# Optimization experiments

Hardware: AMD Instinct MI355X
Metric: run time of the kernel (lower is better)

Reference implementation:

```python
import jax, jax.numpy as jnp
import numpy as np

B, S, D, H, E, FF = 4, 1024, 1024, 16, 8, 2048
DH = D // H
EPS = 1e-5


def layer_norm(x, g, b):
    mu = jnp.mean(x, axis=-1, keepdims=True)
    var = jnp.mean(jnp.square(x - mu), axis=-1, keepdims=True)
    return (x - mu) * jax.lax.rsqrt(var + EPS) * g + b


def setup_inputs() -> dict:
    key = jax.random.key(0)
    ks = jax.random.split(key, 16)
    s = 1.0 / np.sqrt(D)
    sf = 1.0 / np.sqrt(FF)
    return {
        "src": jax.random.normal(ks[0], (B, S, D), jnp.float32),
        "src_key_padding_mask": jnp.zeros((B, S), jnp.bool_),
        "in_proj_w": jax.random.normal(ks[1], (3 * D, D), jnp.float32) * s,
        "in_proj_b": jnp.zeros((3 * D,), jnp.float32),
        "out_proj_w": jax.random.normal(ks[2], (D, D), jnp.float32) * s,
        "out_proj_b": jnp.zeros((D,), jnp.float32),
        "gate_w": jax.random.normal(ks[3], (E, D), jnp.float32) * s,
        "gate_b": jnp.zeros((E,), jnp.float32),
        "w1": jax.random.normal(ks[4], (E, D, FF), jnp.float32) * s,
        "b1": jnp.zeros((E, FF), jnp.float32),
        "w2": jax.random.normal(ks[5], (E, FF, D), jnp.float32) * sf,
        "b2": jnp.zeros((E, D), jnp.float32),
        "ln1_g": jnp.ones((D,), jnp.float32),
        "ln1_b": jnp.zeros((D,), jnp.float32),
        "ln2_g": jnp.ones((D,), jnp.float32),
        "ln2_b": jnp.zeros((D,), jnp.float32),
    }


def _encoder_layer(src, kpm, in_proj_w, in_proj_b, out_proj_w, out_proj_b,
                   gate_w, gate_b, w1, b1, w2, b2, ln1_g, ln1_b, ln2_g, ln2_b):
    # --- multi-head self-attention (batch_first, key_padding_mask) ---
    qkv = src @ in_proj_w.T + in_proj_b                       # [B,S,3D]
    q, k, v = jnp.split(qkv, 3, axis=-1)
    q = q.reshape(B, S, H, DH).transpose(0, 2, 1, 3)          # [B,H,S,DH]
    k = k.reshape(B, S, H, DH).transpose(0, 2, 1, 3)
    v = v.reshape(B, S, H, DH).transpose(0, 2, 1, 3)
    scores = jnp.einsum('bhqd,bhkd->bhqk', q, k) / np.sqrt(DH)
    scores = jnp.where(kpm[:, None, None, :], -jnp.inf, scores)
    attn = jax.nn.softmax(scores, axis=-1)
    ctx = jnp.einsum('bhqk,bhkd->bhqd', attn, v)              # [B,H,S,DH]
    ctx = ctx.transpose(0, 2, 1, 3).reshape(B, S, D)
    attn_out = ctx @ out_proj_w.T + out_proj_b

    x = layer_norm(src + attn_out, ln1_g, ln1_b)

    # --- MoE feedforward: softmax gate, dense weighted mixture of experts ---
    gates = jax.nn.softmax(x @ gate_w.T + gate_b, axis=-1)    # [B,S,E]
    h = jax.nn.relu(jnp.einsum('bsd,edf->bsef', x, w1) + b1)  # [B,S,E,FF]
    y = jnp.einsum('bsef,efd->bsed', h, w2) + b2              # [B,S,E,D]
    ff = jnp.einsum('bse,bsed->bsd', gates, y)

    return layer_norm(x + ff, ln2_g, ln2_b)


def reference(src, src_key_padding_mask, in_proj_w, in_proj_b, out_proj_w,
              out_proj_b, gate_w, gate_b, w1, b1, w2, b2,
              ln1_g, ln1_b, ln2_g, ln2_b):
    return _encoder_layer(src, src_key_padding_mask, in_proj_w, in_proj_b,
                          out_proj_w, out_proj_b, gate_w, gate_b,
                          w1, b1, w2, b2, ln1_g, ln1_b, ln2_g, ln2_b)
```

## Files before the change

kernel.cpp:

```cpp
#include <hip/hip_runtime.h>
#include <math.h>

#define B_   4
#define S_   1024
#define D_   1024
#define H_   16
#define DH_  64
#define E_   8
#define FF_  2048
#define M_   (B_ * S_)
#define EPS_ 1e-5f

typedef _Float16 f16;
typedef f16  f16x8 __attribute__((ext_vector_type(8)));
typedef f16  f16x4 __attribute__((ext_vector_type(4)));
typedef float f32x4 __attribute__((ext_vector_type(4)));

__device__ __forceinline__ void gl_lds16(const f16* g, f16* l) {
  __builtin_amdgcn_global_load_lds(
      (const __attribute__((address_space(1))) void*)g,
      (__attribute__((address_space(3))) void*)l, 16, 0, 0);
}

__global__ __launch_bounds__(256) void cvt_f16(
    const float* __restrict__ in, f16* __restrict__ out, int n8) {
  int i = blockIdx.x * 256 + threadIdx.x;
  if (i >= n8) return;
  float4 u = ((const float4*)in)[(size_t)i * 2];
  float4 v = ((const float4*)in)[(size_t)i * 2 + 1];
  f16x8 o;
  o[0] = (f16)u.x; o[1] = (f16)u.y; o[2] = (f16)u.z; o[3] = (f16)u.w;
  o[4] = (f16)v.x; o[5] = (f16)v.y; o[6] = (f16)v.z; o[7] = (f16)v.w;
  *(f16x8*)&out[(size_t)i * 8] = o;
}

__global__ __launch_bounds__(256) void transpose_cvt(
    const float* __restrict__ in, f16* __restrict__ out, int R, int C) {
  __shared__ float t[32][33];
  const size_t pl = (size_t)blockIdx.z * R * C;
  in += pl; out += pl;
  const int c0 = blockIdx.x * 32, r0 = blockIdx.y * 32;
  const int tx = threadIdx.x & 31, ty = threadIdx.x >> 5;
#pragma unroll
  for (int i = 0; i < 4; ++i)
    t[ty + 8 * i][tx] = in[(size_t)(r0 + ty + 8 * i) * C + c0 + tx];
  __syncthreads();
#pragma unroll
  for (int i = 0; i < 4; ++i)
    out[(size_t)(c0 + ty + 8 * i) * R + r0 + tx] = (f16)t[tx][ty + 8 * i];
}

#define MODE_F32  0
#define MODE_QKV  1
#define MODE_MOE1 2
#define MODE_MOE2 3

template<int MODE>
__global__ __launch_bounds__(256) void gemm16(
    const f16* __restrict__ A, const f16* __restrict__ B,
    const float* __restrict__ bias, const float* __restrict__ gates,
    float* __restrict__ Cf, f16* __restrict__ Ch,
    int N, int K, int e0, int ecnt, int accum) {
  __shared__ f16 Ah[128 * 64];
  __shared__ f16 Bh[128 * 64];
  const int tid = threadIdx.x;
  const int wid = tid >> 6, lane = tid & 63;
  const int wm = wid >> 1, wn = wid & 1;
  const int r16 = lane & 15, kg = lane >> 4;
  const int m0 = blockIdx.y * 128, n0 = blockIdx.x * 128;
  const int z = blockIdx.z;
  const int srow = lane >> 3;
  const int sslot = (lane & 7) ^ srow;

  const f16* Bb = B;
  f16* Chb = Ch;
  float* Cfb = Cf;
  if (MODE == MODE_MOE1) { Bb += (size_t)z * N * K; Chb += (size_t)z * M_ * N; }
  if (MODE == MODE_MOE2) { Cfb += (size_t)z * M_ * N; }

  char* AhB = (char*)Ah;
  char* BhB = (char*)Bh;
  const int rbA = (wm * 64 + r16) * 128;
  const int rbB = (wn * 64 + r16) * 128;
  const int sw0 = ((0 + kg) ^ (r16 & 7)) << 4;
  const int sw1 = ((4 + kg) ^ (r16 & 7)) << 4;

  f32x4 acc[4][4] = {};
  const int nloop = (MODE == MODE_MOE2) ? ecnt : 1;
  for (int ee = 0; ee < nloop; ++ee) {
    const f16* Ae = A;
    const f16* Be = Bb;
    if (MODE == MODE_MOE2) {
      Ae = A  + (size_t)(z * ecnt + ee) * M_ * K;
      Be = B  + (size_t)(z * ecnt + ee) * N * K;
    }
    const f16* ApL = Ae + (size_t)(m0 + wid * 32 + srow) * K + sslot * 8;
    const f16* BpL = Be + (size_t)(n0 + wid * 32 + srow) * K + sslot * 8;
    for (int k0 = 0; k0 < K; k0 += 64) {
      __syncthreads();
#pragma unroll
      for (int ia = 0; ia < 4; ++ia)
        gl_lds16(ApL + (size_t)ia * 8 * K + k0, (f16*)(AhB + (wid * 4 + ia) * 1024));
#pragma unroll
      for (int ib = 0; ib < 4; ++ib)
        gl_lds16(BpL + (size_t)ib * 8 * K + k0, (f16*)(BhB + (wid * 4 + ib) * 1024));
      __syncthreads();
#pragma unroll
      for (int ks = 0; ks < 2; ++ks) {
        const int sw = ks ? sw1 : sw0;
        f16x8 af[4], bf[4];
#pragma unroll
        for (int i = 0; i < 4; ++i)
          af[i] = *(const f16x8*)(AhB + rbA + i * 2048 + sw);
#pragma unroll
        for (int j = 0; j < 4; ++j)
          bf[j] = *(const f16x8*)(BhB + rbB + j * 2048 + sw);
#pragma unroll
        for (int i = 0; i < 4; ++i)
#pragma unroll
          for (int j = 0; j < 4; ++j)
            acc[i][j] = __builtin_amdgcn_mfma_f32_16x16x32_f16(
                af[i], bf[j], acc[i][j], 0, 0, 0);
      }
    }
  }
#pragma unroll
  for (int i = 0; i < 4; ++i) {
#pragma unroll
    for (int r = 0; r < 4; ++r) {
      const int row = m0 + wm * 64 + i * 16 + kg * 4 + r;
      float gsc = 0.f;
      if (MODE == MODE_MOE1) gsc = gates[(size_t)row * E_ + e0 + z];
#pragma unroll
      for (int j = 0; j < 4; ++j) {
        const int col = n0 + wn * 64 + j * 16 + r16;
        float v = acc[i][j][r];
        if (MODE == MODE_F32) {
          Cfb[(size_t)row * N + col] = v + bias[col];
        } else if (MODE == MODE_QKV) {
          Chb[(size_t)row * N + col] = (f16)(v + bias[col]);
        } else if (MODE == MODE_MOE1) {
          float t = fmaxf(v + bias[(size_t)(e0 + z) * N + col], 0.f) * gsc;
          Chb[(size_t)row * N + col] = (f16)t;
        } else {
          float o = v;
          if (accum) o += Cfb[(size_t)row * N + col];
          Cfb[(size_t)row * N + col] = o;
        }
      }
    }
  }
}

__global__ __launch_bounds__(256) void attn_kernel(
    const f16* __restrict__ qkv, const unsigned char* __restrict__ kpm,
    f16* __restrict__ ctxh) {
  __shared__ f16 Qs[64][72];
  __shared__ f16 Ks[64][72];
  __shared__ f16 VTs[64][72];
  __shared__ f16 Ps[4][16][72];
  const int tid = threadIdx.x;
  const int w = tid >> 6, lane = tid & 63;
  const int cx = lane & 15, qg = lane >> 4;
  const int qt = blockIdx.x, h = blockIdx.y, b = blockIdx.z;
  const size_t base = (size_t)b * S_ * (3 * D_);
  const f16* Qg = qkv + base + h * 64;
  const f16* Kg = qkv + base + D_ + h * 64;
  const f16* Vg = qkv + base + 2 * D_ + h * 64;
  const int lr = tid >> 2, lc = (tid & 3) * 16;

  {
    const f16* sp = &Qg[(size_t)(qt * 64 + lr) * (3 * D_) + lc];
    *(f16x8*)&Qs[lr][lc]     = *(const f16x8*)&sp[0];
    *(f16x8*)&Qs[lr][lc + 8] = *(const f16x8*)&sp[8];
  }
  __syncthreads();
  f16x8 aq0 = *(const f16x8*)&Qs[w * 16 + cx][qg * 8];
  f16x8 aq1 = *(const f16x8*)&Qs[w * 16 + cx][32 + qg * 8];

  f32x4 accO[4] = {};
  float mrun[4], lrun[4];
#pragma unroll
  for (int r = 0; r < 4; ++r) { mrun[r] = -__builtin_inff(); lrun[r] = 0.f; }

  for (int kt = 0; kt < 16; ++kt) {
    __syncthreads();
    {
      const f16* ksp = &Kg[(size_t)(kt * 64 + lr) * (3 * D_) + lc];
      const f16* vsp = &Vg[(size_t)(kt * 64 + lr) * (3 * D_) + lc];
      *(f16x8*)&Ks[lr][lc]     = *(const f16x8*)&ksp[0];
      *(f16x8*)&Ks[lr][lc + 8] = *(const f16x8*)&ksp[8];
      f16x8 v0 = *(const f16x8*)&vsp[0];
      f16x8 v1 = *(const f16x8*)&vsp[8];
#pragma unroll
      for (int j = 0; j < 8; ++j) {
        VTs[lc + j][lr]     = v0[j];
        VTs[lc + 8 + j][lr] = v1[j];
      }
    }
    __syncthreads();
    f32x4 s[4];
#pragma unroll
    for (int t = 0; t < 4; ++t) {
      f16x8 bk0 = *(const f16x8*)&Ks[t * 16 + cx][qg * 8];
      f16x8 bk1 = *(const f16x8*)&Ks[t * 16 + cx][32 + qg * 8];
      f32x4 zz = {};
      zz = __builtin_amdgcn_mfma_f32_16x16x32_f16(aq0, bk0, zz, 0, 0, 0);
      zz = __builtin_amdgcn_mfma_f32_16x16x32_f16(aq1, bk1, zz, 0, 0, 0);
      s[t] = zz;
    }
    const unsigned char* mp = &kpm[(size_t)b * S_ + kt * 64];
    bool mk[4];
#pragma unroll
    for (int t = 0; t < 4; ++t) mk[t] = mp[t * 16 + cx] != 0;
#pragma unroll
    for (int r = 0; r < 4; ++r) {
      float sv[4];
#pragma unroll
      for (int t = 0; t < 4; ++t)
        sv[t] = mk[t] ? -__builtin_inff() : s[t][r] * 0.125f;
      float mx = fmaxf(fmaxf(sv[0], sv[1]), fmaxf(sv[2], sv[3]));
#pragma unroll
      for (int mm = 1; mm < 16; mm <<= 1) mx = fmaxf(mx, __shfl_xor(mx, mm, 64));
      float mnew = fmaxf(mrun[r], mx);
      float al = (mrun[r] == -__builtin_inff()) ? 0.f : __expf(mrun[r] - mnew);
      float ps = 0.f;
#pragma unroll
      for (int t = 0; t < 4; ++t) {
        float p = __expf(sv[t] - mnew);
        Ps[w][qg * 4 + r][t * 16 + cx] = (f16)p;
        ps += p;
      }
#pragma unroll
      for (int mm = 1; mm < 16; mm <<= 1) ps += __shfl_xor(ps, mm, 64);
      lrun[r] = lrun[r] * al + ps;
      mrun[r] = mnew;
#pragma unroll
      for (int t = 0; t < 4; ++t) accO[t][r] *= al;
    }
    f16x8 ap0 = *(const f16x8*)&Ps[w][cx][qg * 8];
    f16x8 ap1 = *(const f16x8*)&Ps[w][cx][32 + qg * 8];
#pragma unroll
    for (int td = 0; td < 4; ++td) {
      f16x8 bv0 = *(const f16x8*)&VTs[td * 16 + cx][qg * 8];
      f16x8 bv1 = *(const f16x8*)&VTs[td * 16 + cx][32 + qg * 8];
      accO[td] = __builtin_amdgcn_mfma_f32_16x16x32_f16(ap0, bv0, accO[td], 0, 0, 0);
      accO[td] = __builtin_amdgcn_mfma_f32_16x16x32_f16(ap1, bv1, accO[td], 0, 0, 0);
    }
  }
  f16* outp = ctxh + (size_t)b * S_ * D_ + h * 64;
#pragma unroll
  for (int r = 0; r < 4; ++r) {
    float inv = 1.f / lrun[r];
    const size_t rofs = (size_t)(qt * 64 + w * 16 + qg * 4 + r) * D_;
#pragma unroll
    for (int td = 0; td < 4; ++td)
      outp[rofs + td * 16 + cx] = (f16)(accO[td][r] * inv);
  }
}

__global__ __launch_bounds__(256) void add_ln(
    const float* __restrict__ x1, const float* __restrict__ parts, int nparts,
    const float* __restrict__ gates, const float* __restrict__ b2,
    const float* __restrict__ g, const float* __restrict__ bta,
    float* __restrict__ out, f16* __restrict__ outh) {
  __shared__ float red[4];
  const int row = blockIdx.x, tid = threadIdx.x;
  const size_t off = (size_t)row * D_ + tid * 4;
  float4 a = *(const float4*)&x1[off];
  float v[4] = {a.x, a.y, a.z, a.w};
  for (int p = 0; p < nparts; ++p) {
    float4 c = *(const float4*)&parts[(size_t)p * M_ * D_ + off];
    v[0] += c.x; v[1] += c.y; v[2] += c.z; v[3] += c.w;
  }
  if (gates) {
#pragma unroll
    for (int e = 0; e < E_; ++e) {
      float ge = gates[(size_t)row * E_ + e];
      float4 bb = *(const float4*)&b2[(size_t)e * D_ + tid * 4];
      v[0] += ge * bb.x; v[1] += ge * bb.y; v[2] += ge * bb.z; v[3] += ge * bb.w;
    }
  }
  float p = v[0] + v[1] + v[2] + v[3];
#pragma unroll
  for (int mm = 32; mm >= 1; mm >>= 1) p += __shfl_xor(p, mm, 64);
  if ((tid & 63) == 0) red[tid >> 6] = p;
  __syncthreads();
  float mu = (red[0] + red[1] + red[2] + red[3]) * (1.f / D_);
  __syncthreads();
  float d0 = v[0] - mu, d1 = v[1] - mu, d2 = v[2] - mu, d3 = v[3] - mu;
  float p2 = d0 * d0 + d1 * d1 + d2 * d2 + d3 * d3;
#pragma unroll
  for (int mm = 32; mm >= 1; mm >>= 1) p2 += __shfl_xor(p2, mm, 64);
  if ((tid & 63) == 0) red[tid >> 6] = p2;
  __syncthreads();
  float var = (red[0] + red[1] + red[2] + red[3]) * (1.f / D_);
  float sc = rsqrtf(var + EPS_);
  float4 gg = *(const float4*)&g[tid * 4];
  float4 bb = *(const float4*)&bta[tid * 4];
  float o0 = d0 * sc * gg.x + bb.x;
  float o1 = d1 * sc * gg.y + bb.y;
  float o2 = d2 * sc * gg.z + bb.z;
  float o3 = d3 * sc * gg.w + bb.w;
  float4 o = {o0, o1, o2, o3};
  *(float4*)&out[off] = o;
  if (outh) {
    f16x4 oh; oh[0] = (f16)o0; oh[1] = (f16)o1; oh[2] = (f16)o2; oh[3] = (f16)o3;
    *(f16x4*)&outh[off] = oh;
  }
}

__global__ __launch_bounds__(256) void gate_kernel(
    const float* __restrict__ x, const float* __restrict__ gw,
    const float* __restrict__ gb, float* __restrict__ gates) {
  const int lane = threadIdx.x & 63;
  const int row = blockIdx.x * 4 + (threadIdx.x >> 6);
  const float* xr = x + (size_t)row * D_;
  float a[E_] = {};
#pragma unroll
  for (int c = 0; c < 4; ++c) {
    float4 xv = *(const float4*)&xr[lane * 16 + c * 4];
#pragma unroll
    for (int e = 0; e < E_; ++e) {
      float4 wv = *(const float4*)&gw[(size_t)e * D_ + lane * 16 + c * 4];
      a[e] += xv.x * wv.x + xv.y * wv.y + xv.z * wv.z + xv.w * wv.w;
    }
  }
#pragma unroll
  for (int e = 0; e < E_; ++e) {
#pragma unroll
    for (int mm = 1; mm < 64; mm <<= 1) a[e] += __shfl_xor(a[e], mm, 64);
    a[e] += gb[e];
  }
  if (lane == 0) {
    float mx = a[0];
#pragma unroll
    for (int e = 1; e < E_; ++e) mx = fmaxf(mx, a[e]);
    float pr[E_], sum = 0.f;
#pragma unroll
    for (int e = 0; e < E_; ++e) { pr[e] = __expf(a[e] - mx); sum += pr[e]; }
    float inv = 1.f / sum;
#pragma unroll
    for (int e = 0; e < E_; ++e) gates[(size_t)row * E_ + e] = pr[e] * inv;
  }
}

extern "C" void kernel_launch(void* const* d_in, const int* in_sizes, int n_in,
                              void* d_out, int out_size, void* d_ws, size_t ws_size,
                              hipStream_t stream) {
  (void)in_sizes; (void)n_in; (void)out_size;
  const float* src         = (const float*)d_in[0];
  const unsigned char* kpm = (const unsigned char*)d_in[1];
  const float* in_proj_w   = (const float*)d_in[2];
  const float* in_proj_b   = (const float*)d_in[3];
  const float* out_proj_w  = (const float*)d_in[4];
  const float* out_proj_b  = (const float*)d_in[5];
  const float* gate_w      = (const float*)d_in[6];
  const float* gate_b      = (const float*)d_in[7];
  const float* w1          = (const float*)d_in[8];
  const float* b1          = (const float*)d_in[9];
  const float* w2          = (const float*)d_in[10];
  const float* b2          = (const float*)d_in[11];
  const float* ln1_g       = (const float*)d_in[12];
  const float* ln1_b       = (const float*)d_in[13];
  const float* ln2_g       = (const float*)d_in[14];
  const float* ln2_b       = (const float*)d_in[15];
  float* out = (float*)d_out;

  const size_t MD4 = (size_t)M_ * D_ * 4;
  const size_t MD2 = (size_t)M_ * D_ * 2;
  const size_t persist = MD4 + MD2 + (size_t)M_ * E_ * 4;
  const size_t wfull   = (size_t)E_ * D_ * FF_ * 2;
  const size_t phaseA  = MD2 + (size_t)3 * D_ * D_ * 2 + (size_t)D_ * D_ * 2
                       + (size_t)M_ * 3 * D_ * 2 + MD2 + MD4;
  const size_t phaseBb = (size_t)E_ * M_ * FF_ * 2 + 4 * MD4;
  const size_t bigBytes = persist + 2 * wfull + (phaseBb > phaseA ? phaseBb : phaseA);

  char* p = (char*)d_ws;
  float* x_  = (float*)p;  p += MD4;
  f16*   x_h = (f16*)p;    p += MD2;
  float* gts = (float*)p;  p += (size_t)M_ * E_ * 4;
  const bool big = ws_size >= bigBytes;
  f16 *w1t = nullptr, *w2t = nullptr;
  if (big) { w1t = (f16*)p; p += wfull; w2t = (f16*)p; p += wfull; }
  char* region = p;
  f16*   src_h = (f16*)region;
  f16*   ipw   = (f16*)(region + MD2);
  f16*   opw   = (f16*)(region + MD2 + 6291456);
  f16*   qkvh  = (f16*)(region + MD2 + 6291456 + 2097152);
  f16*   ctxh  = (f16*)(region + MD2 + 6291456 + 2097152 + 25165824);
  float* aout  = (float*)(region + MD2 + 6291456 + 2097152 + 25165824 + MD2);

  dim3 blk(256);
  cvt_f16<<<2048, blk, 0, stream>>>(src, src_h, M_ * D_ / 8);
  cvt_f16<<<1536, blk, 0, stream>>>(in_proj_w, ipw, 3 * D_ * D_ / 8);
  cvt_f16<<<512,  blk, 0, stream>>>(out_proj_w, opw, D_ * D_ / 8);
  if (big) {
    transpose_cvt<<<dim3(FF_ / 32, D_ / 32, E_), blk, 0, stream>>>(w1, w1t, D_, FF_);
    transpose_cvt<<<dim3(D_ / 32, FF_ / 32, E_), blk, 0, stream>>>(w2, w2t, FF_, D_);
  }
  gemm16<MODE_QKV><<<dim3(24, 32), blk, 0, stream>>>(
      src_h, ipw, in_proj_b, nullptr, nullptr, qkvh, 3 * D_, D_, 0, 0, 0);
  attn_kernel<<<dim3(S_ / 64, H_, B_), blk, 0, stream>>>(qkvh, kpm, ctxh);
  gemm16<MODE_F32><<<dim3(8, 32), blk, 0, stream>>>(
      ctxh, opw, out_proj_b, nullptr, aout, nullptr, D_, D_, 0, 0, 0);
  add_ln<<<M_, blk, 0, stream>>>(src, aout, 1, nullptr, nullptr, ln1_g, ln1_b, x_, x_h);
  gate_kernel<<<M_ / 4, blk, 0, stream>>>(x_, gate_w, gate_b, gts);
  if (big) {
    f16*   h_h = (f16*)region;
    float* ff  = (float*)(region + (size_t)E_ * M_ * FF_ * 2);
    gemm16<MODE_MOE1><<<dim3(16, 32, 8), blk, 0, stream>>>(
        x_h, w1t, b1, gts, nullptr, h_h, FF_, D_, 0, 0, 0);
    gemm16<MODE_MOE2><<<dim3(8, 32, 4), blk, 0, stream>>>(
        h_h, w2t, nullptr, nullptr, ff, nullptr, D_, FF_, 0, 2, 0);
    add_ln<<<M_, blk, 0, stream>>>(x_, ff, 4, gts, b2, ln2_g, ln2_b, out, nullptr);
  } else {
    f16*   w1tp = (f16*)region;
    f16*   w2tp = (f16*)(region + 8388608);
    f16*   h_p  = (f16*)(region + 16777216);
    float* ffp  = (float*)(region + 16777216 + 33554432);
    for (int pp = 0; pp < 4; ++pp) {
      transpose_cvt<<<dim3(FF_ / 32, D_ / 32, 2), blk, 0, stream>>>(
          w1 + (size_t)pp * 2 * D_ * FF_, w1tp, D_, FF_);
      transpose_cvt<<<dim3(D_ / 32, FF_ / 32, 2), blk, 0, stream>>>(
          w2 + (size_t)pp * 2 * FF_ * D_, w2tp, FF_, D_);
      gemm16<MODE_MOE1><<<dim3(16, 32, 2), blk, 0, stream>>>(
          x_h, w1tp, b1, gts, nullptr, h_p, FF_, D_, 2 * pp, 0, 0);
      gemm16<MODE_MOE2><<<dim3(8, 32, 2), blk, 0, stream>>>(
          h_p, w2tp, nullptr, nullptr, ffp, nullptr, D_, FF_, 0, 1, pp > 0);
    }
    add_ln<<<M_, blk, 0, stream>>>(x_, ffp, 2, gts, b2, ln2_g, ln2_b, out, nullptr);
  }
}
```

Before: 789.5 us.

## Add 256x256 double-buffered GEMM, split-K MoE down-proj with fp16 partials

Adds a new 512-thread GEMM kernel with 256x256 tiles, BK=32, double-buffered direct-to-LDS loads and setprio around MFMA bursts. It replaces the QKV and MoE GEMMs. The MoE second GEMM is split four ways along K and accumulates fp16 partials across experts, and the attention output is stored in fp16. The big-workspace path that transposed all expert weights at once is removed, so experts are always processed two at a time in a smaller buffer. Accumulating partial sums in fp16 across 8 experts risks precision loss, and the smaller K-split launches may underuse the GPU.

Measured after the change: 988.4 us. 1.25x slower.

```diff
diff --git a/kernel.cpp b/kernel.cpp
--- a/kernel.cpp
+++ b/kernel.cpp
@@ -21,6 +21,11 @@
       (const __attribute__((address_space(1))) void*)g,
       (__attribute__((address_space(3))) void*)l, 16, 0, 0);
 }
+
+#define MODE_F32  0
+#define MODE_QKV  1
+#define MODE_MOE1 2
+#define MODE_MOE2 3
 
 __global__ __launch_bounds__(256) void cvt_f16(
     const float* __restrict__ in, f16* __restrict__ out, int n8) {
@@ -37,8 +42,8 @@
 __global__ __launch_bounds__(256) void transpose_cvt(
     const float* __restrict__ in, f16* __restrict__ out, int R, int C) {
   __shared__ float t[32][33];
-  const size_t pl = (size_t)blockIdx.z * R * C;
-  in += pl; out += pl;
+  in  += (size_t)blockIdx.z * R * C;
+  out += (size_t)blockIdx.z * R * C;
   const int c0 = blockIdx.x * 32, r0 = blockIdx.y * 32;
   const int tx = threadIdx.x & 31, ty = threadIdx.x >> 5;
 #pragma unroll
@@ -50,17 +55,117 @@
     out[(size_t)(c0 + ty + 8 * i) * R + r0 + tx] = (f16)t[tx][ty + 8 * i];
 }
 
-#define MODE_F32  0
-#define MODE_QKV  1
-#define MODE_MOE1 2
-#define MODE_MOE2 3
+template<int MODE>
+__global__ __launch_bounds__(512, 2) void gemm2(
+    const f16* __restrict__ A, int lda,
+    const f16* __restrict__ B, int ldb,
+    const float* __restrict__ bias, const float* __restrict__ gates,
+    f16* __restrict__ C, int N, int NT, int e0, int accum) {
+  __shared__ f16 Ab[2 * 256 * 32];
+  __shared__ f16 Bb[2 * 256 * 32];
+  const int tid = threadIdx.x;
+  const int wid = tid >> 6, lane = tid & 63;
+  const int wm = wid >> 2, wn = wid & 3;
+  const int r16 = lane & 15, kg = lane >> 4;
+  const int m0 = blockIdx.y * 256, n0 = blockIdx.x * 256;
+  const int z = blockIdx.z;
+
+  const f16* Ap = A;
+  const f16* Bp = B;
+  f16* Cp = C;
+  if (MODE == MODE_MOE1) {
+    Bp += (size_t)z * N * 1024;
+    Cp += (size_t)z * M_ * N;
+  }
+  if (MODE == MODE_MOE2) {
+    Ap += z * 512;
+    Bp += z * 512;
+    Cp += (size_t)z * M_ * N;
+  }
+
+  const int srow = tid >> 2;
+  const int sg   = (tid & 3) ^ ((tid >> 3) & 3);
+  const f16* Asrc = Ap + (size_t)(m0 + srow) * lda + sg * 8;
+  const f16* Bsrc = Bp + (size_t)(n0 + srow) * ldb + sg * 8;
+  char* AbC = (char*)Ab;
+  char* BbC = (char*)Bb;
+  const int ldsW = wid * 1024;
+
+#define STAGE2(tt, bb)                                                         \
+  {                                                                            \
+    gl_lds16(Asrc + (tt) * 32,                   (f16*)(AbC + (bb) * 16384 + ldsW));        \
+    gl_lds16(Asrc + (size_t)128 * lda + (tt) * 32, (f16*)(AbC + (bb) * 16384 + 8192 + ldsW)); \
+    gl_lds16(Bsrc + (tt) * 32,                   (f16*)(BbC + (bb) * 16384 + ldsW));        \
+    gl_lds16(Bsrc + (size_t)128 * ldb + (tt) * 32, (f16*)(BbC + (bb) * 16384 + 8192 + ldsW)); \
+  }
+
+  const int sswz = (kg ^ ((r16 >> 1) & 3)) * 16;
+  const int aoff = (wm * 128 + r16) * 64 + sswz;
+  const int boff = (wn * 64 + r16) * 64 + sswz;
+
+  f32x4 acc[8][4] = {};
+  STAGE2(0, 0);
+  for (int t = 0; t < NT; ++t) {
+    const int b = t & 1;
+    if (t + 1 < NT) {
+      STAGE2(t + 1, b ^ 1);
+      asm volatile("s_waitcnt vmcnt(4)" ::: "memory");
+    } else {
+      asm volatile("s_waitcnt vmcnt(0)" ::: "memory");
+    }
+    __builtin_amdgcn_sched_barrier(0);
+    __builtin_amdgcn_s_barrier();
+    f16x8 af[8], bf[4];
+#pragma unroll
+    for (int i = 0; i < 8; ++i)
+      af[i] = *(const f16x8*)(AbC + b * 16384 + aoff + i * 1024);
+#pragma unroll
+    for (int j = 0; j < 4; ++j)
+      bf[j] = *(const f16x8*)(BbC + b * 16384 + boff + j * 1024);
+    __builtin_amdgcn_s_setprio(1);
+#pragma unroll
+    for (int i = 0; i < 8; ++i)
+#pragma unroll
+      for (int j = 0; j < 4; ++j)
+        acc[i][j] = __builtin_amdgcn_mfma_f32_16x16x32_f16(
+            af[i], bf[j], acc[i][j], 0, 0, 0);
+    __builtin_amdgcn_s_setprio(0);
+    asm volatile("" ::: "memory");
+    __builtin_amdgcn_sched_barrier(0);
+    __builtin_amdgcn_s_barrier();
+  }
+#undef STAGE2
+
+#pragma unroll
+  for (int i = 0; i < 8; ++i) {
+#pragma unroll
+    for (int r = 0; r < 4; ++r) {
+      const int row = m0 + wm * 128 + i * 16 + kg * 4 + r;
+      float gsc = 0.f;
+      if (MODE == MODE_MOE1) gsc = gates[(size_t)row * E_ + e0 + z];
+#pragma unroll
+      for (int j = 0; j < 4; ++j) {
+        const int col = n0 + wn * 64 + j * 16 + r16;
+        float v = acc[i][j][r];
+        if (MODE == MODE_QKV) {
+          Cp[(size_t)row * N + col] = (f16)(v + bias[col]);
+        } else if (MODE == MODE_MOE1) {
+          float tv = fmaxf(v + bias[(size_t)z * N + col], 0.f) * gsc;
+          Cp[(size_t)row * N + col] = (f16)tv;
+        } else {
+          float o = v;
+          if (accum) o += (float)Cp[(size_t)row * N + col];
+          Cp[(size_t)row * N + col] = (f16)o;
+        }
+      }
+    }
+  }
+}
 
 template<int MODE>
 __global__ __launch_bounds__(256) void gemm16(
     const f16* __restrict__ A, const f16* __restrict__ B,
-    const float* __restrict__ bias, const float* __restrict__ gates,
-    float* __restrict__ Cf, f16* __restrict__ Ch,
-    int N, int K, int e0, int ecnt, int accum) {
+    const float* __restrict__ bias, f16* __restrict__ Ch, int N, int K) {
   __shared__ f16 Ah[128 * 64];
   __shared__ f16 Bh[128 * 64];
   const int tid = threadIdx.x;
@@ -68,15 +173,8 @@
   const int wm = wid >> 1, wn = wid & 1;
   const int r16 = lane & 15, kg = lane >> 4;
   const int m0 = blockIdx.y * 128, n0 = blockIdx.x * 128;
-  const int z = blockIdx.z;
   const int srow = lane >> 3;
   const int sslot = (lane & 7) ^ srow;
-
-  const f16* Bb = B;
-  f16* Chb = Ch;
-  float* Cfb = Cf;
-  if (MODE == MODE_MOE1) { Bb += (size_t)z * N * K; Chb += (size_t)z * M_ * N; }
-  if (MODE == MODE_MOE2) { Cfb += (size_t)z * M_ * N; }
 
   char* AhB = (char*)Ah;
   char* BhB = (char*)Bh;
@@ -86,70 +184,46 @@
   const int sw1 = ((4 + kg) ^ (r16 & 7)) << 4;
 
   f32x4 acc[4][4] = {};
-  const int nloop = (MODE == MODE_MOE2) ? ecnt : 1;
-  for (int ee = 0; ee < nloop; ++ee) {
-    const f16* Ae = A;
-    const f16* Be = Bb;
-    if (MODE == MODE_MOE2) {
-      Ae = A  + (size_t)(z * ecnt + ee) * M_ * K;
-      Be = B  + (size_t)(z * ecnt + ee) * N * K;
-    }
-    const f16* ApL = Ae + (size_t)(m0 + wid * 32 + srow) * K + sslot * 8;
-    const f16* BpL = Be + (size_t)(n0 + wid * 32 + srow) * K + sslot * 8;
-    for (int k0 = 0; k0 < K; k0 += 64) {
-      __syncthreads();
-#pragma unroll
-      for (int ia = 0; ia < 4; ++ia)
-        gl_lds16(ApL + (size_t)ia * 8 * K + k0, (f16*)(AhB + (wid * 4 + ia) * 1024));
-#pragma unroll
-      for (int ib = 0; ib < 4; ++ib)
-        gl_lds16(BpL + (size_t)ib * 8 * K + k0, (f16*)(BhB + (wid * 4 + ib) * 1024));
-      __syncthreads();
-#pragma unroll
-      for (int ks = 0; ks < 2; ++ks) {
-        const int sw = ks ? sw1 : sw0;
-        f16x8 af[4], bf[4];
-#pragma unroll
-        for (int i = 0; i < 4; ++i)
-          af[i] = *(const f16x8*)(AhB + rbA + i * 2048 + sw);
+  const f16* ApL = A + (size_t)(m0 + wid * 32 + srow) * K + sslot * 8;
+  const f16* BpL = B + (size_t)(n0 + wid * 32 + srow) * K + sslot * 8;
+  for (int k0 = 0; k0 < K; k0 += 64) {
+    __syncthreads();
+#pragma unroll
+    for (int ia = 0; ia < 4; ++ia)
+      gl_lds16(ApL + (size_t)ia * 8 * K + k0, (f16*)(AhB + (wid * 4 + ia) * 1024));
+#pragma unroll
+    for (int ib = 0; ib < 4; ++ib)
+      gl_lds16(BpL + (size_t)ib * 8 * K + k0, (f16*)(BhB + (wid * 4 + ib) * 1024));
+    __syncthreads();
+#pragma unroll
+    for (int ks = 0; ks < 2; ++ks) {
+      const int sw = ks ? sw1 : sw0;
+      f16x8 af[4], bf[4];
+#pragma unroll
+      for (int i = 0; i < 4; ++i)
+        af[i] = *(const f16x8*)(AhB + rbA + i * 2048 + sw);
+#pragma unroll
+      for (int j = 0; j < 4; ++j)
+        bf[j] = *(const f16x8*)(BhB + rbB + j * 2048 + sw);
+#pragma unroll
+      for (int i = 0; i < 4; ++i)
 #pragma unroll
         for (int j = 0; j < 4; ++j)
-          bf[j] = *(const f16x8*)(BhB + rbB + j * 2048 + sw);
-#pragma unroll
-        for (int i = 0; i < 4; ++i)
-#pragma unroll
-          for (int j = 0; j < 4; ++j)
-            acc[i][j] = __builtin_amdgcn_mfma_f32_16x16x32_f16(
-                af[i], bf[j], acc[i][j], 0, 0, 0);
-      }
-    }
-  }
-#pragma unroll
-  for (int i = 0; i < 4; ++i) {
+          acc[i][j] = __builtin_amdgcn_mfma_f32_16x16x32_f16(
+              af[i], bf[j], acc[i][j], 0, 0, 0);
+    }
+  }
+#pragma unroll
+  for (int i = 0; i < 4; ++i)
 #pragma unroll
     for (int r = 0; r < 4; ++r) {
       const int row = m0 + wm * 64 + i * 16 + kg * 4 + r;
-      float gsc = 0.f;
-      if (MODE == MODE_MOE1) gsc = gates[(size_t)row * E_ + e0 + z];
 #pragma unroll
       for (int j = 0; j < 4; ++j) {
         const int col = n0 + wn * 64 + j * 16 + r16;
-        float v = acc[i][j][r];
-        if (MODE == MODE_F32) {
-          Cfb[(size_t)row * N + col] = v + bias[col];
-        } else if (MODE == MODE_QKV) {
-          Chb[(size_t)row * N + col] = (f16)(v + bias[col]);
-        } else if (MODE == MODE_MOE1) {
-          float t = fmaxf(v + bias[(size_t)(e0 + z) * N + col], 0.f) * gsc;
-          Chb[(size_t)row * N + col] = (f16)t;
-        } else {
-          float o = v;
-          if (accum) o += Cfb[(size_t)row * N + col];
-          Cfb[(size_t)row * N + col] = o;
-        }
+        Ch[(size_t)row * N + col] = (f16)(acc[i][j][r] + bias[col]);
       }
     }
-  }
 }
 
 __global__ __launch_bounds__(256) void attn_kernel(
@@ -260,7 +334,7 @@
 }
 
 __global__ __launch_bounds__(256) void add_ln(
-    const float* __restrict__ x1, const float* __restrict__ parts, int nparts,
+    const float* __restrict__ x1, const f16* __restrict__ parts, int nparts,
     const float* __restrict__ gates, const float* __restrict__ b2,
     const float* __restrict__ g, const float* __restrict__ bta,
     float* __restrict__ out, f16* __restrict__ outh) {
@@ -270,8 +344,9 @@
   float4 a = *(const float4*)&x1[off];
   float v[4] = {a.x, a.y, a.z, a.w};
   for (int p = 0; p < nparts; ++p) {
-    float4 c = *(const float4*)&parts[(size_t)p * M_ * D_ + off];
-    v[0] += c.x; v[1] += c.y; v[2] += c.z; v[3] += c.w;
+    f16x4 c = *(const f16x4*)&parts[(size_t)p * M_ * D_ + off];
+    v[0] += (float)c[0]; v[1] += (float)c[1];
+    v[2] += (float)c[2]; v[3] += (float)c[3];
   }
   if (gates) {
 #pragma unroll
@@ -348,7 +423,7 @@
 extern "C" void kernel_launch(void* const* d_in, const int* in_sizes, int n_in,
                               void* d_out, int out_size, void* d_ws, size_t ws_size,
                               hipStream_t stream) {
-  (void)in_sizes; (void)n_in; (void)out_size;
+  (void)in_sizes; (void)n_in; (void)out_size; (void)ws_size;
   const float* src         = (const float*)d_in[0];
   const unsigned char* kpm = (const unsigned char*)d_in[1];
   const float* in_proj_w   = (const float*)d_in[2];
@@ -367,68 +442,48 @@
   const float* ln2_b       = (const float*)d_in[15];
   float* out = (float*)d_out;
 
-  const size_t MD4 = (size_t)M_ * D_ * 4;
-  const size_t MD2 = (size_t)M_ * D_ * 2;
-  const size_t persist = MD4 + MD2 + (size_t)M_ * E_ * 4;
-  const size_t wfull   = (size_t)E_ * D_ * FF_ * 2;
-  const size_t phaseA  = MD2 + (size_t)3 * D_ * D_ * 2 + (size_t)D_ * D_ * 2
-                       + (size_t)M_ * 3 * D_ * 2 + MD2 + MD4;
-  const size_t phaseBb = (size_t)E_ * M_ * FF_ * 2 + 4 * MD4;
-  const size_t bigBytes = persist + 2 * wfull + (phaseBb > phaseA ? phaseBb : phaseA);
-
   char* p = (char*)d_ws;
-  float* x_  = (float*)p;  p += MD4;
-  f16*   x_h = (f16*)p;    p += MD2;
+  float* x_  = (float*)p;  p += (size_t)M_ * D_ * 4;
+  f16*   x_h = (f16*)p;    p += (size_t)M_ * D_ * 2;
   float* gts = (float*)p;  p += (size_t)M_ * E_ * 4;
-  const bool big = ws_size >= bigBytes;
-  f16 *w1t = nullptr, *w2t = nullptr;
-  if (big) { w1t = (f16*)p; p += wfull; w2t = (f16*)p; p += wfull; }
   char* region = p;
+
   f16*   src_h = (f16*)region;
-  f16*   ipw   = (f16*)(region + MD2);
-  f16*   opw   = (f16*)(region + MD2 + 6291456);
-  f16*   qkvh  = (f16*)(region + MD2 + 6291456 + 2097152);
-  f16*   ctxh  = (f16*)(region + MD2 + 6291456 + 2097152 + 25165824);
-  float* aout  = (float*)(region + MD2 + 6291456 + 2097152 + 25165824 + MD2);
-
-  dim3 blk(256);
+  f16*   ipw   = (f16*)(region + 8388608);
+  f16*   opw   = (f16*)(region + 8388608 + 6291456);
+  f16*   qkvh  = (f16*)(region + 8388608 + 6291456 + 2097152);
+  f16*   ctxh  = (f16*)(region + 8388608 + 6291456 + 2097152 + 25165824);
+  f16*   aouth = src_h;
+
+  f16*   wts = (f16*)region;
+  f16*   h2  = (f16*)(region + 8388608);
+  f16*   ff4 = (f16*)(region + 8388608 + 33554432);
+
+  dim3 blk(256), blk2(512);
   cvt_f16<<<2048, blk, 0, stream>>>(src, src_h, M_ * D_ / 8);
   cvt_f16<<<1536, blk, 0, stream>>>(in_proj_w, ipw, 3 * D_ * D_ / 8);
   cvt_f16<<<512,  blk, 0, stream>>>(out_proj_w, opw, D_ * D_ / 8);
-  if (big) {
-    transpose_cvt<<<dim3(FF_ / 32, D_ / 32, E_), blk, 0, stream>>>(w1, w1t, D_, FF_);
-    transpose_cvt<<<dim3(D_ / 32, FF_ / 32, E_), blk, 0, stream>>>(w2, w2t, FF_, D_);
-  }
-  gemm16<MODE_QKV><<<dim3(24, 32), blk, 0, stream>>>(
-      src_h, ipw, in_proj_b, nullptr, nullptr, qkvh, 3 * D_, D_, 0, 0, 0);
+  gemm2<MODE_QKV><<<dim3(12, 16), blk2, 0, stream>>>(
+      src_h, D_, ipw, D_, in_proj_b, nullptr, qkvh, 3 * D_, 32, 0, 0);
   attn_kernel<<<dim3(S_ / 64, H_, B_), blk, 0, stream>>>(qkvh, kpm, ctxh);
-  gemm16<MODE_F32><<<dim3(8, 32), blk, 0, stream>>>(
-      ctxh, opw, out_proj_b, nullptr, aout, nullptr, D_, D_, 0, 0, 0);
-  add_ln<<<M_, blk, 0, stream>>>(src, aout, 1, nullptr, nullptr, ln1_g, ln1_b, x_, x_h);
+  gemm16<MODE_QKV><<<dim3(8, 32), blk, 0, stream>>>(
+      ctxh, opw, out_proj_b, aouth, D_, D_);
+  add_ln<<<M_, blk, 0, stream>>>(src, aouth, 1, nullptr, nullptr,
+                                 ln1_g, ln1_b, x_, x_h);
   gate_kernel<<<M_ / 4, blk, 0, stream>>>(x_, gate_w, gate_b, gts);
-  if (big) {
-    f16*   h_h = (f16*)region;
-    float* ff  = (float*)(region + (size_t)E_ * M_ * FF_ * 2);
-    gemm16<MODE_MOE1><<<dim3(16, 32, 8), blk, 0, stream>>>(
-        x_h, w1t, b1, gts, nullptr, h_h, FF_, D_, 0, 0, 0);
-    gemm16<MODE_MOE2><<<dim3(8, 32, 4), blk, 0, stream>>>(
-        h_h, w2t, nullptr, nullptr, ff, nullptr, D_, FF_, 0, 2, 0);
-    add_ln<<<M_, blk, 0, stream>>>(x_, ff, 4, gts, b2, ln2_g, ln2_b, out, nullptr);
-  } else {
-    f16*   w1tp = (f16*)region;
-    f16*   w2tp = (f16*)(region + 8388608);
-    f16*   h_p  = (f16*)(region + 16777216);
-    float* ffp  = (float*)(region + 16777216 + 33554432);
-    for (int pp = 0; pp < 4; ++pp) {
-      transpose_cvt<<<dim3(FF_ / 32, D_ / 32, 2), blk, 0, stream>>>(
-          w1 + (size_t)pp * 2 * D_ * FF_, w1tp, D_, FF_);
-      transpose_cvt<<<dim3(D_ / 32, FF_ / 32, 2), blk, 0, stream>>>(
-          w2 + (size_t)pp * 2 * FF_ * D_, w2tp, FF_, D_);
-      gemm16<MODE_MOE1><<<dim3(16, 32, 2), blk, 0, stream>>>(
-          x_h, w1tp, b1, gts, nullptr, h_p, FF_, D_, 2 * pp, 0, 0);
-      gemm16<MODE_MOE2><<<dim3(8, 32, 2), blk, 0, stream>>>(
-          h_p, w2tp, nullptr, nullptr, ffp, nullptr, D_, FF_, 0, 1, pp > 0);
-    }
-    add_ln<<<M_, blk, 0, stream>>>(x_, ffp, 2, gts, b2, ln2_g, ln2_b, out, nullptr);
-  }
-}
+  for (int pp = 0; pp < 4; ++pp) {
+    const int e0 = 2 * pp;
+    transpose_cvt<<<dim3(FF_ / 32, D_ / 32, 2), blk, 0, stream>>>(
+        w1 + (size_t)e0 * D_ * FF_, wts, D_, FF_);
+    gemm2<MODE_MOE1><<<dim3(8, 16, 2), blk2, 0, stream>>>(
+        x_h, D_, wts, D_, b1 + (size_t)e0 * FF_, gts, h2, FF_, 32, e0, 0);
+    transpose_cvt<<<dim3(D_ / 32, FF_ / 32, 2), blk, 0, stream>>>(
+        w2 + (size_t)e0 * FF_ * D_, wts, FF_, D_);
+    for (int e2 = 0; e2 < 2; ++e2) {
+      gemm2<MODE_MOE2><<<dim3(4, 16, 4), blk2, 0, stream>>>(
+          h2 + (size_t)e2 * M_ * FF_, FF_, wts + (size_t)e2 * D_ * FF_, FF_,
+          nullptr, nullptr, ff4, D_, 16, 0, (pp > 0 || e2 > 0) ? 1 : 0);
+    }
+  }
+  add_ln<<<M_, blk, 0, stream>>>(x_, ff4, 4, gts, b2, ln2_g, ln2_b, out, nullptr);
+}
```
